# Kernel tuning notes

Hardware: AMD Instinct MI355X
Metric: run time of the kernel (lower is better)

## Reference

```python
import jax, jax.numpy as jnp
import numpy as np

N, E, F_IN, H, K = 50000, 800000, 64, 128, 4


def setup_inputs() -> dict:
    key = jax.random.key(0)
    k0, k1, k2, k3 = jax.random.split(key, 4)
    features = jax.random.normal(k0, (N, F_IN), dtype=jnp.float32)
    edge_index = jax.random.randint(k1, (2, E), 0, N, dtype=jnp.int32)
    # ChebConv parameters: one [F_IN, H] weight per Chebyshev order + shared bias
    cheb_w = jax.random.normal(k2, (K, F_IN, H), dtype=jnp.float32) * 0.05
    cheb_b = jnp.zeros((H,), dtype=jnp.float32)
    # final Linear(H, 1)
    final_w = jax.random.normal(k3, (H, 1), dtype=jnp.float32) * 0.05
    final_b = jnp.zeros((1,), dtype=jnp.float32)
    return dict(features=features, edge_index=edge_index, cheb_w=cheb_w,
                cheb_b=cheb_b, final_w=final_w, final_b=final_b)


def _cheb_conv(x, edge_index, w, b):
    # PyG ChebConv, sym normalization, lambda_max = 2.0, no self-loops in input:
    # L_hat = (2/lambda_max) * (I - D^-1/2 A D^-1/2) - I = -D^-1/2 A D^-1/2
    row, col = edge_index[0], edge_index[1]
    n = x.shape[0]
    deg = jax.ops.segment_sum(jnp.ones((row.shape[0],), dtype=x.dtype), row,
                              num_segments=n)
    dinv = jnp.where(deg > 0, jax.lax.rsqrt(jnp.maximum(deg, 1e-12)), 0.0)
    ew = -dinv[row] * dinv[col]  # [E] normalized (negated) edge weights

    def spmm(z):  # L_hat @ z via gather-multiply-scatter
        return jax.ops.segment_sum(z[col] * ew[:, None], row, num_segments=n)

    Tx0 = x
    out = Tx0 @ w[0]
    Tx1 = spmm(Tx0)
    if w.shape[0] > 1:
        out = out + Tx1 @ w[1]
    for k in range(2, w.shape[0]):  # Chebyshev recursion T_k = 2 L T_{k-1} - T_{k-2}
        Tx2 = 2.0 * spmm(Tx1) - Tx0
        out = out + Tx2 @ w[k]
        Tx0, Tx1 = Tx1, Tx2
    return out + b


def reference(features, edge_index, cheb_w, cheb_b, final_w, final_b):
    h = jnp.tanh(_cheb_conv(features, edge_index, cheb_w, cheb_b))  # [N, H]
    return (h @ final_w + final_b).reshape(-1)  # [N]
```

## Files before the change

### kernel.cpp

```cpp
#include <hip/hip_runtime.h>
#include <hip/hip_fp16.h>
#include <math.h>


#define FIN 64
#define HDIM 128

typedef _Float16 half8 __attribute__((ext_vector_type(8)));
typedef float f32x4 __attribute__((ext_vector_type(4)));

union U16 { uint4 u; __half2 h2[4]; half8 h8; };

__global__ void count_deg(const int* __restrict__ row, int* __restrict__ deg, int E) {
    int e = blockIdx.x * blockDim.x + threadIdx.x;
    if (e < E) atomicAdd(&deg[row[e]], 1);
}

__global__ void make_dinv(const int* __restrict__ deg, float* __restrict__ dinv, int n) {
    int i = blockIdx.x * blockDim.x + threadIdx.x;
    if (i < n) {
        int d = deg[i];
        dinv[i] = (d > 0) ? rsqrtf((float)d) : 0.f;
    }
}

__global__ void cvt_feat(const float4* __restrict__ src, uint4* __restrict__ dst, int n8) {
    int i = blockIdx.x * blockDim.x + threadIdx.x;
    if (i >= n8) return;
    float4 a = src[i * 2], b = src[i * 2 + 1];
    U16 v;
    v.h2[0] = __float22half2_rn(make_float2(a.x, a.y));
    v.h2[1] = __float22half2_rn(make_float2(a.z, a.w));
    v.h2[2] = __float22half2_rn(make_float2(b.x, b.y));
    v.h2[3] = __float22half2_rn(make_float2(b.z, b.w));
    dst[i] = v.u;
}

__global__ void make_bfrag(const float* __restrict__ W, uint4* __restrict__ bfrag) {
    int t = blockIdx.x * blockDim.x + threadIdx.x;
    if (t >= 8 * 8 * 64) return;
    int lane = t & 63;
    int ht = (t >> 6) & 7;
    int kk = t >> 9;
    int h = ht * 16 + (lane & 15);
    int kb = kk * 32 + (lane >> 4) * 8;
    U16 v;
#pragma unroll
    for (int j = 0; j < 4; ++j) {
        float a = W[(kb + 2 * j) * HDIM + h];
        float b = W[(kb + 2 * j + 1) * HDIM + h];
        v.h2[j] = __float22half2_rn(make_float2(a, b));
    }
    bfrag[t] = v.u;
}

__global__ void scan_local(const int* __restrict__ in, int* __restrict__ out,
                           int* __restrict__ bsum, int n) {
    __shared__ int buf[1024];
    int tid = threadIdx.x;
    int gid = blockIdx.x * 1024 + tid;
    int v = (gid < n) ? in[gid] : 0;
    int x = v;
    buf[tid] = x;
    __syncthreads();
    for (int off = 1; off < 1024; off <<= 1) {
        int t = (tid >= off) ? buf[tid - off] : 0;
        __syncthreads();
        x += t;
        buf[tid] = x;
        __syncthreads();
    }
    if (gid < n) out[gid] = x - v;
    if (tid == 1023) bsum[blockIdx.x] = x;
}

__global__ void scan_bsums(int* bsum, int nb) {
    if (blockIdx.x == 0 && threadIdx.x == 0) {
        int acc = 0;
        for (int b = 0; b < nb; ++b) { int t = bsum[b]; bsum[b] = acc; acc += t; }
    }
}

__global__ void scan_finish(int* __restrict__ rowptr, const int* __restrict__ bsum,
                            int* __restrict__ cursor, int n, int E) {
    int i = blockIdx.x * blockDim.x + threadIdx.x;
    if (i < n) {
        int v = rowptr[i] + bsum[i >> 10];
        rowptr[i] = v;
        cursor[i] = v;
    } else if (i == n) {
        rowptr[n] = E;
    }
}

__global__ void scatter_edges(const int* __restrict__ row, const int* __restrict__ col,
                              const float* __restrict__ dinv, int* __restrict__ cursor,
                              int2* __restrict__ epk, int E) {
    int e = blockIdx.x * blockDim.x + threadIdx.x;
    if (e < E) {
        int r = row[e], c = col[e];
        int p = atomicAdd(&cursor[r], 1);
        float w = -dinv[r] * dinv[c];
        epk[p] = make_int2(c, __float_as_int(w));
    }
}

__global__ __launch_bounds__(256) void spmm_h(
        const int* __restrict__ rowptr, const int2* __restrict__ epk,
        const uint4* __restrict__ in8, const uint4* __restrict__ prev8,
        float scale, uint4* __restrict__ out8, int n) {
    int lane = threadIdx.x & 63;
    int wid = (blockIdx.x * blockDim.x + threadIdx.x) >> 6;
    int li = lane & 7, g = lane >> 3;
    int r = wid * 8 + g;
    if (r >= n) return;
    int s = rowptr[r], e = rowptr[r + 1];
    float acc[8];
#pragma unroll
    for (int j = 0; j < 8; ++j) acc[j] = 0.f;
    int p = s;
    for (; p + 4 <= e; p += 4) {
        int2 m0 = epk[p], m1 = epk[p + 1], m2 = epk[p + 2], m3 = epk[p + 3];
        U16 v0, v1, v2, v3;
        v0.u = in8[(size_t)m0.x * 8 + li];
        v1.u = in8[(size_t)m1.x * 8 + li];
        v2.u = in8[(size_t)m2.x * 8 + li];
        v3.u = in8[(size_t)m3.x * 8 + li];
        float w0 = __int_as_float(m0.y), w1 = __int_as_float(m1.y);
        float w2 = __int_as_float(m2.y), w3 = __int_as_float(m3.y);
#pragma unroll
        for (int j = 0; j < 4; ++j) {
            float2 f0 = __half22float2(v0.h2[j]);
            float2 f1 = __half22float2(v1.h2[j]);
            float2 f2 = __half22float2(v2.h2[j]);
            float2 f3 = __half22float2(v3.h2[j]);
            acc[2 * j]     = fmaf(w0, f0.x, acc[2 * j]);
            acc[2 * j + 1] = fmaf(w0, f0.y, acc[2 * j + 1]);
            acc[2 * j]     = fmaf(w1, f1.x, acc[2 * j]);
            acc[2 * j + 1] = fmaf(w1, f1.y, acc[2 * j + 1]);
            acc[2 * j]     = fmaf(w2, f2.x, acc[2 * j]);
            acc[2 * j + 1] = fmaf(w2, f2.y, acc[2 * j + 1]);
            acc[2 * j]     = fmaf(w3, f3.x, acc[2 * j]);
            acc[2 * j + 1] = fmaf(w3, f3.y, acc[2 * j + 1]);
        }
    }
    for (; p < e; ++p) {
        int2 m0 = epk[p];
        U16 v0;
        v0.u = in8[(size_t)m0.x * 8 + li];
        float w0 = __int_as_float(m0.y);
#pragma unroll
        for (int j = 0; j < 4; ++j) {
            float2 f0 = __half22float2(v0.h2[j]);
            acc[2 * j]     = fmaf(w0, f0.x, acc[2 * j]);
            acc[2 * j + 1] = fmaf(w0, f0.y, acc[2 * j + 1]);
        }
    }
    if (prev8) {
        U16 pv;
        pv.u = prev8[(size_t)r * 8 + li];
#pragma unroll
        for (int j = 0; j < 4; ++j) {
            float2 f = __half22float2(pv.h2[j]);
            acc[2 * j]     = fmaf(scale, acc[2 * j], -f.x);
            acc[2 * j + 1] = fmaf(scale, acc[2 * j + 1], -f.y);
        }
    }
    U16 res;
#pragma unroll
    for (int j = 0; j < 4; ++j)
        res.h2[j] = __float22half2_rn(make_float2(acc[2 * j], acc[2 * j + 1]));
    out8[(size_t)r * 8 + li] = res.u;
}

__device__ inline float tanh_fast(float x) {
    x = fmaxf(-10.f, fminf(10.f, x));
    float e = __expf(2.f * x);
    return (e - 1.f) / (e + 1.f);
}

__global__ __launch_bounds__(256) void gemm_mfma(
        const uint4* __restrict__ tx0, const uint4* __restrict__ tx1,
        const uint4* __restrict__ tx2, const uint4* __restrict__ tx3,
        const uint4* __restrict__ bfrag,
        const float* __restrict__ cheb_b, const float* __restrict__ fw,
        const float* __restrict__ fb, float* __restrict__ out, int n) {
    int tid = threadIdx.x;
    int lane = tid & 63;
    int wave = tid >> 6;
    int q = lane >> 4, m = lane & 15;
    int node_base = blockIdx.x * 64 + wave * 16;
    int node = node_base + m;
    size_t nd = (node < n) ? (size_t)node : 0;

    f32x4 acc[8];
#pragma unroll
    for (int t = 0; t < 8; ++t) acc[t] = (f32x4){0.f, 0.f, 0.f, 0.f};

    const uint4* txs[4] = {tx0, tx1, tx2, tx3};
#pragma unroll
    for (int kk = 0; kk < 8; ++kk) {
        U16 av;
        av.u = txs[kk >> 1][nd * 8 + (kk & 1) * 4 + q];
#pragma unroll
        for (int ht = 0; ht < 8; ++ht) {
            U16 bv;
            bv.u = bfrag[(kk * 8 + ht) * 64 + lane];
            acc[ht] = __builtin_amdgcn_mfma_f32_16x16x32_f16(av.h8, bv.h8, acc[ht], 0, 0, 0);
        }
    }

    float s[4] = {0.f, 0.f, 0.f, 0.f};
#pragma unroll
    for (int ht = 0; ht < 8; ++ht) {
        int h = ht * 16 + m;
        float cb = cheb_b[h];
        float fv = fw[h];
#pragma unroll
        for (int r = 0; r < 4; ++r)
            s[r] = fmaf(tanh_fast(acc[ht][r] + cb), fv, s[r]);
    }
#pragma unroll
    for (int r = 0; r < 4; ++r) {
        for (int msk = 1; msk < 16; msk <<= 1)
            s[r] += __shfl_xor(s[r], msk, 64);
    }
    if (m == 0) {
        float fb0 = fb[0];
#pragma unroll
        for (int r = 0; r < 4; ++r) {
            int o = node_base + q * 4 + r;
            if (o < n) out[o] = s[r] + fb0;
        }
    }
}

extern "C" void kernel_launch(void* const* d_in, const int* in_sizes, int n_in,
                              void* d_out, int out_size, void* d_ws, size_t ws_size,
                              hipStream_t stream) {
    const float* features = (const float*)d_in[0];
    const int*   edge_index = (const int*)d_in[1];
    const float* cheb_w  = (const float*)d_in[2];
    const float* cheb_b  = (const float*)d_in[3];
    const float* final_w = (const float*)d_in[4];
    const float* final_b = (const float*)d_in[5];
    int N = in_sizes[0] / FIN;
    int E = in_sizes[1] / 2;
    const int* row = edge_index;
    const int* col = edge_index + E;

    char* p = (char*)d_ws;
    auto alloc = [&](size_t bytes) {
        char* r = p;
        p += (bytes + 255) & ~(size_t)255;
        return r;
    };
    int*   deg    = (int*)alloc((size_t)N * 4);
    float* dinv   = (float*)alloc((size_t)N * 4);
    int*   rowptr = (int*)alloc((size_t)(N + 1) * 4);
    int*   cursor = (int*)alloc((size_t)N * 4);
    int*   bsum   = (int*)alloc(1024 * 4);
    int2*  epk    = (int2*)alloc((size_t)E * 8);
    uint4* feath  = (uint4*)alloc((size_t)N * FIN * 2);
    uint4* tx1h   = (uint4*)alloc((size_t)N * FIN * 2);
    uint4* tx2h   = (uint4*)alloc((size_t)N * FIN * 2);
    uint4* tx3h   = (uint4*)alloc((size_t)N * FIN * 2);
    uint4* bfrag  = (uint4*)alloc(4096 * 16);

    hipMemsetAsync(deg, 0, (size_t)N * 4, stream);
    count_deg<<<(E + 255) / 256, 256, 0, stream>>>(row, deg, E);
    make_dinv<<<(N + 255) / 256, 256, 0, stream>>>(deg, dinv, N);
    int n8 = N * FIN / 8;
    cvt_feat<<<(n8 + 255) / 256, 256, 0, stream>>>((const float4*)features, feath, n8);
    make_bfrag<<<16, 256, 0, stream>>>(cheb_w, bfrag);
    int nb = (N + 1023) / 1024;
    scan_local<<<nb, 1024, 0, stream>>>(deg, rowptr, bsum, N);
    scan_bsums<<<1, 64, 0, stream>>>(bsum, nb);
    scan_finish<<<(N + 1 + 255) / 256, 256, 0, stream>>>(rowptr, bsum, cursor, N, E);
    scatter_edges<<<(E + 255) / 256, 256, 0, stream>>>(row, col, dinv, cursor, epk, E);

    int waves = (N + 7) / 8;
    int spmm_blocks = (waves * 64 + 255) / 256;
    spmm_h<<<spmm_blocks, 256, 0, stream>>>(rowptr, epk, feath, nullptr, 1.f, tx1h, N);
    spmm_h<<<spmm_blocks, 256, 0, stream>>>(rowptr, epk, tx1h, feath, 2.f, tx2h, N);
    spmm_h<<<spmm_blocks, 256, 0, stream>>>(rowptr, epk, tx2h, tx1h, 2.f, tx3h, N);

    gemm_mfma<<<(N + 63) / 64, 256, 0, stream>>>(feath, tx1h, tx2h, tx3h, bfrag,
                                                 cheb_b, final_w, final_b,
                                                 (float*)d_out, N);
}
```

Baseline: 231.7 us.

## Split SpMM rows across edge halves and feature halves with shuffle reduction

```diff
diff --git a/kernel.cpp b/kernel.cpp
--- a/kernel.cpp
+++ b/kernel.cpp
@@ -109,23 +109,33 @@
         const int* __restrict__ rowptr, const int2* __restrict__ epk,
         const uint4* __restrict__ in8, const uint4* __restrict__ prev8,
         float scale, uint4* __restrict__ out8, int n) {
-    int lane = threadIdx.x & 63;
-    int wid = (blockIdx.x * blockDim.x + threadIdx.x) >> 6;
-    int li = lane & 7, g = lane >> 3;
-    int r = wid * 8 + g;
+    int half = blockIdx.x & 1;
+    int bid = blockIdx.x >> 1;
+    int tid = threadIdx.x;
+    int lane = tid & 63;
+    int wave = bid * 4 + (tid >> 6);
+    int g = lane >> 3;
+    int sub = (lane >> 2) & 1;
+    int li = lane & 3;
+    int r = wave * 8 + g;
     if (r >= n) return;
     int s = rowptr[r], e = rowptr[r + 1];
+    int mid = s + ((e - s + 1) >> 1);
+    int p = sub ? mid : s;
+    int pe = sub ? e : mid;
+    int fo = half * 4 + li;
+
     float acc[8];
 #pragma unroll
     for (int j = 0; j < 8; ++j) acc[j] = 0.f;
-    int p = s;
-    for (; p + 4 <= e; p += 4) {
+
+    for (; p + 4 <= pe; p += 4) {
         int2 m0 = epk[p], m1 = epk[p + 1], m2 = epk[p + 2], m3 = epk[p + 3];
         U16 v0, v1, v2, v3;
-        v0.u = in8[(size_t)m0.x * 8 + li];
-        v1.u = in8[(size_t)m1.x * 8 + li];
-        v2.u = in8[(size_t)m2.x * 8 + li];
-        v3.u = in8[(size_t)m3.x * 8 + li];
+        v0.u = in8[(size_t)m0.x * 8 + fo];
+        v1.u = in8[(size_t)m1.x * 8 + fo];
+        v2.u = in8[(size_t)m2.x * 8 + fo];
+        v3.u = in8[(size_t)m3.x * 8 + fo];
         float w0 = __int_as_float(m0.y), w1 = __int_as_float(m1.y);
         float w2 = __int_as_float(m2.y), w3 = __int_as_float(m3.y);
 #pragma unroll
@@ -144,10 +154,10 @@
             acc[2 * j + 1] = fmaf(w3, f3.y, acc[2 * j + 1]);
         }
     }
-    for (; p < e; ++p) {
+    for (; p < pe; ++p) {
         int2 m0 = epk[p];
         U16 v0;
-        v0.u = in8[(size_t)m0.x * 8 + li];
+        v0.u = in8[(size_t)m0.x * 8 + fo];
         float w0 = __int_as_float(m0.y);
 #pragma unroll
         for (int j = 0; j < 4; ++j) {
@@ -156,21 +166,29 @@
             acc[2 * j + 1] = fmaf(w0, f0.y, acc[2 * j + 1]);
         }
     }
-    if (prev8) {
-        U16 pv;
-        pv.u = prev8[(size_t)r * 8 + li];
-#pragma unroll
-        for (int j = 0; j < 4; ++j) {
-            float2 f = __half22float2(pv.h2[j]);
-            acc[2 * j]     = fmaf(scale, acc[2 * j], -f.x);
-            acc[2 * j + 1] = fmaf(scale, acc[2 * j + 1], -f.y);
-        }
-    }
-    U16 res;
-#pragma unroll
-    for (int j = 0; j < 4; ++j)
-        res.h2[j] = __float22half2_rn(make_float2(acc[2 * j], acc[2 * j + 1]));
-    out8[(size_t)r * 8 + li] = res.u;
+#pragma unroll
+    for (int j = 0; j < 8; ++j) acc[j] += __shfl_xor(acc[j], 4, 64);
+
+    if (sub == 0) {
+        if (prev8) {
+            U16 pv;
+            pv.u = prev8[(size_t)r * 8 + fo];
+#pragma unroll
+            for (int j = 0; j < 4; ++j) {
+                float2 f = __half22float2(pv.h2[j]);
+                acc[2 * j]     = fmaf(scale, acc[2 * j], -f.x);
+                acc[2 * j + 1] = fmaf(scale, acc[2 * j + 1], -f.y);
+            }
+        } else {
+#pragma unroll
+            for (int j = 0; j < 8; ++j) acc[j] *= scale;
+        }
+        U16 res;
+#pragma unroll
+        for (int j = 0; j < 4; ++j)
+            res.h2[j] = __float22half2_rn(make_float2(acc[2 * j], acc[2 * j + 1]));
+        out8[(size_t)r * 8 + fo] = res.u;
+    }
 }
 
 __device__ inline float tanh_fast(float x) {
@@ -279,11 +297,11 @@
     scan_finish<<<(N + 1 + 255) / 256, 256, 0, stream>>>(rowptr, bsum, cursor, N, E);
     scatter_edges<<<(E + 255) / 256, 256, 0, stream>>>(row, col, dinv, cursor, epk, E);
 
-    int waves = (N + 7) / 8;
-    int spmm_blocks = (waves * 64 + 255) / 256;
-    spmm_h<<<spmm_blocks, 256, 0, stream>>>(rowptr, epk, feath, nullptr, 1.f, tx1h, N);
-    spmm_h<<<spmm_blocks, 256, 0, stream>>>(rowptr, epk, tx1h, feath, 2.f, tx2h, N);
-    spmm_h<<<spmm_blocks, 256, 0, stream>>>(rowptr, epk, tx2h, tx1h, 2.f, tx3h, N);
+    int blocks_per_half = (N + 31) / 32;
+    int spmm_grid = blocks_per_half * 2;
+    spmm_h<<<spmm_grid, 256, 0, stream>>>(rowptr, epk, feath, nullptr, 1.f, tx1h, N);
+    spmm_h<<<spmm_grid, 256, 0, stream>>>(rowptr, epk, tx1h, feath, 2.f, tx2h, N);
+    spmm_h<<<spmm_grid, 256, 0, stream>>>(rowptr, epk, tx2h, tx1h, 2.f, tx3h, N);
 
     gemm_mfma<<<(N + 63) / 64, 256, 0, stream>>>(feath, tx1h, tx2h, tx3h, bfrag,
                                                  cheb_b, final_w, final_b,
```

Result: slower. 261.0 us (+12.7%).

## Factor symmetric normalization out of SpMM and store column-only CSR

Applied to the files above, without the earlier changes.

```diff
diff --git a/kernel.cpp b/kernel.cpp
--- a/kernel.cpp
+++ b/kernel.cpp
@@ -24,16 +24,23 @@
     }
 }
 
-__global__ void cvt_feat(const float4* __restrict__ src, uint4* __restrict__ dst, int n8) {
+__global__ void cvt_feat(const float4* __restrict__ src, const float* __restrict__ dinv,
+                         uint4* __restrict__ dsth, uint4* __restrict__ dsts, int n8) {
     int i = blockIdx.x * blockDim.x + threadIdx.x;
     if (i >= n8) return;
+    float d = dinv[i >> 3];
     float4 a = src[i * 2], b = src[i * 2 + 1];
-    U16 v;
+    U16 v, vs;
     v.h2[0] = __float22half2_rn(make_float2(a.x, a.y));
     v.h2[1] = __float22half2_rn(make_float2(a.z, a.w));
     v.h2[2] = __float22half2_rn(make_float2(b.x, b.y));
     v.h2[3] = __float22half2_rn(make_float2(b.z, b.w));
-    dst[i] = v.u;
+    vs.h2[0] = __float22half2_rn(make_float2(d * a.x, d * a.y));
+    vs.h2[1] = __float22half2_rn(make_float2(d * a.z, d * a.w));
+    vs.h2[2] = __float22half2_rn(make_float2(d * b.x, d * b.y));
+    vs.h2[3] = __float22half2_rn(make_float2(d * b.z, d * b.w));
+    dsth[i] = v.u;
+    dsts[i] = vs.u;
 }
 
 __global__ void make_bfrag(const float* __restrict__ W, uint4* __restrict__ bfrag) {
@@ -93,22 +100,24 @@
     }
 }
 
-__global__ void scatter_edges(const int* __restrict__ row, const int* __restrict__ col,
-                              const float* __restrict__ dinv, int* __restrict__ cursor,
-                              int2* __restrict__ epk, int E) {
+__global__ void scatter_pass(const int* __restrict__ row, const int* __restrict__ col,
+                             int* __restrict__ cursor, int* __restrict__ col_s,
+                             int E, int r_lo, int r_hi) {
     int e = blockIdx.x * blockDim.x + threadIdx.x;
     if (e < E) {
-        int r = row[e], c = col[e];
-        int p = atomicAdd(&cursor[r], 1);
-        float w = -dinv[r] * dinv[c];
-        epk[p] = make_int2(c, __float_as_int(w));
-    }
-}
-
-__global__ __launch_bounds__(256) void spmm_h(
-        const int* __restrict__ rowptr, const int2* __restrict__ epk,
-        const uint4* __restrict__ in8, const uint4* __restrict__ prev8,
-        float scale, uint4* __restrict__ out8, int n) {
+        int r = row[e];
+        if (r >= r_lo && r < r_hi) {
+            int p = atomicAdd(&cursor[r], 1);
+            col_s[p] = col[e];
+        }
+    }
+}
+
+__global__ __launch_bounds__(256) void spmm_g(
+        const int* __restrict__ rowptr, const int* __restrict__ cols,
+        const uint4* __restrict__ ins, const uint4* __restrict__ prevu,
+        const float* __restrict__ dinv, float two,
+        uint4* __restrict__ outu, uint4* __restrict__ outs, int n) {
     int lane = threadIdx.x & 63;
     int wid = (blockIdx.x * blockDim.x + threadIdx.x) >> 6;
     int li = lane & 7, g = lane >> 3;
@@ -119,58 +128,61 @@
 #pragma unroll
     for (int j = 0; j < 8; ++j) acc[j] = 0.f;
     int p = s;
-    for (; p + 4 <= e; p += 4) {
-        int2 m0 = epk[p], m1 = epk[p + 1], m2 = epk[p + 2], m3 = epk[p + 3];
-        U16 v0, v1, v2, v3;
-        v0.u = in8[(size_t)m0.x * 8 + li];
-        v1.u = in8[(size_t)m1.x * 8 + li];
-        v2.u = in8[(size_t)m2.x * 8 + li];
-        v3.u = in8[(size_t)m3.x * 8 + li];
-        float w0 = __int_as_float(m0.y), w1 = __int_as_float(m1.y);
-        float w2 = __int_as_float(m2.y), w3 = __int_as_float(m3.y);
-#pragma unroll
-        for (int j = 0; j < 4; ++j) {
-            float2 f0 = __half22float2(v0.h2[j]);
-            float2 f1 = __half22float2(v1.h2[j]);
-            float2 f2 = __half22float2(v2.h2[j]);
-            float2 f3 = __half22float2(v3.h2[j]);
-            acc[2 * j]     = fmaf(w0, f0.x, acc[2 * j]);
-            acc[2 * j + 1] = fmaf(w0, f0.y, acc[2 * j + 1]);
-            acc[2 * j]     = fmaf(w1, f1.x, acc[2 * j]);
-            acc[2 * j + 1] = fmaf(w1, f1.y, acc[2 * j + 1]);
-            acc[2 * j]     = fmaf(w2, f2.x, acc[2 * j]);
-            acc[2 * j + 1] = fmaf(w2, f2.y, acc[2 * j + 1]);
-            acc[2 * j]     = fmaf(w3, f3.x, acc[2 * j]);
-            acc[2 * j + 1] = fmaf(w3, f3.y, acc[2 * j + 1]);
+    for (; p + 8 <= e; p += 8) {
+        int c[8];
+#pragma unroll
+        for (int j = 0; j < 8; ++j) c[j] = cols[p + j];
+        U16 v[8];
+#pragma unroll
+        for (int j = 0; j < 8; ++j) v[j].u = ins[(size_t)c[j] * 8 + li];
+#pragma unroll
+        for (int j = 0; j < 8; ++j) {
+#pragma unroll
+            for (int t = 0; t < 4; ++t) {
+                float2 f = __half22float2(v[j].h2[t]);
+                acc[2 * t] += f.x;
+                acc[2 * t + 1] += f.y;
+            }
         }
     }
     for (; p < e; ++p) {
-        int2 m0 = epk[p];
-        U16 v0;
-        v0.u = in8[(size_t)m0.x * 8 + li];
-        float w0 = __int_as_float(m0.y);
-#pragma unroll
-        for (int j = 0; j < 4; ++j) {
-            float2 f0 = __half22float2(v0.h2[j]);
-            acc[2 * j]     = fmaf(w0, f0.x, acc[2 * j]);
-            acc[2 * j + 1] = fmaf(w0, f0.y, acc[2 * j + 1]);
-        }
-    }
-    if (prev8) {
+        U16 v;
+        v.u = ins[(size_t)cols[p] * 8 + li];
+#pragma unroll
+        for (int t = 0; t < 4; ++t) {
+            float2 f = __half22float2(v.h2[t]);
+            acc[2 * t] += f.x;
+            acc[2 * t + 1] += f.y;
+        }
+    }
+    float d = dinv[r];
+    float rs = -d * two;
+    float res[8];
+    if (prevu) {
         U16 pv;
-        pv.u = prev8[(size_t)r * 8 + li];
-#pragma unroll
-        for (int j = 0; j < 4; ++j) {
-            float2 f = __half22float2(pv.h2[j]);
-            acc[2 * j]     = fmaf(scale, acc[2 * j], -f.x);
-            acc[2 * j + 1] = fmaf(scale, acc[2 * j + 1], -f.y);
-        }
-    }
-    U16 res;
-#pragma unroll
-    for (int j = 0; j < 4; ++j)
-        res.h2[j] = __float22half2_rn(make_float2(acc[2 * j], acc[2 * j + 1]));
-    out8[(size_t)r * 8 + li] = res.u;
+        pv.u = prevu[(size_t)r * 8 + li];
+#pragma unroll
+        for (int t = 0; t < 4; ++t) {
+            float2 f = __half22float2(pv.h2[t]);
+            res[2 * t]     = fmaf(rs, acc[2 * t], -f.x);
+            res[2 * t + 1] = fmaf(rs, acc[2 * t + 1], -f.y);
+        }
+    } else {
+#pragma unroll
+        for (int j = 0; j < 8; ++j) res[j] = rs * acc[j];
+    }
+    U16 ru;
+#pragma unroll
+    for (int t = 0; t < 4; ++t)
+        ru.h2[t] = __float22half2_rn(make_float2(res[2 * t], res[2 * t + 1]));
+    outu[(size_t)r * 8 + li] = ru.u;
+    if (outs) {
+        U16 rsv;
+#pragma unroll
+        for (int t = 0; t < 4; ++t)
+            rsv.h2[t] = __float22half2_rn(make_float2(d * res[2 * t], d * res[2 * t + 1]));
+        outs[(size_t)r * 8 + li] = rsv.u;
+    }
 }
 
 __device__ inline float tanh_fast(float x) {
@@ -260,10 +272,13 @@
     int*   rowptr = (int*)alloc((size_t)(N + 1) * 4);
     int*   cursor = (int*)alloc((size_t)N * 4);
     int*   bsum   = (int*)alloc(1024 * 4);
-    int2*  epk    = (int2*)alloc((size_t)E * 8);
+    int*   col_s  = (int*)alloc((size_t)E * 4);
     uint4* feath  = (uint4*)alloc((size_t)N * FIN * 2);
+    uint4* feats  = (uint4*)alloc((size_t)N * FIN * 2);
     uint4* tx1h   = (uint4*)alloc((size_t)N * FIN * 2);
+    uint4* tx1s   = (uint4*)alloc((size_t)N * FIN * 2);
     uint4* tx2h   = (uint4*)alloc((size_t)N * FIN * 2);
+    uint4* tx2s   = (uint4*)alloc((size_t)N * FIN * 2);
     uint4* tx3h   = (uint4*)alloc((size_t)N * FIN * 2);
     uint4* bfrag  = (uint4*)alloc(4096 * 16);
 
@@ -271,19 +286,29 @@
     count_deg<<<(E + 255) / 256, 256, 0, stream>>>(row, deg, E);
     make_dinv<<<(N + 255) / 256, 256, 0, stream>>>(deg, dinv, N);
     int n8 = N * FIN / 8;
-    cvt_feat<<<(n8 + 255) / 256, 256, 0, stream>>>((const float4*)features, feath, n8);
+    cvt_feat<<<(n8 + 255) / 256, 256, 0, stream>>>((const float4*)features, dinv,
+                                                   feath, feats, n8);
     make_bfrag<<<16, 256, 0, stream>>>(cheb_w, bfrag);
     int nb = (N + 1023) / 1024;
     scan_local<<<nb, 1024, 0, stream>>>(deg, rowptr, bsum, N);
     scan_bsums<<<1, 64, 0, stream>>>(bsum, nb);
     scan_finish<<<(N + 1 + 255) / 256, 256, 0, stream>>>(rowptr, bsum, cursor, N, E);
-    scatter_edges<<<(E + 255) / 256, 256, 0, stream>>>(row, col, dinv, cursor, epk, E);
-
-    int waves = (N + 7) / 8;
-    int spmm_blocks = (waves * 64 + 255) / 256;
-    spmm_h<<<spmm_blocks, 256, 0, stream>>>(rowptr, epk, feath, nullptr, 1.f, tx1h, N);
-    spmm_h<<<spmm_blocks, 256, 0, stream>>>(rowptr, epk, tx1h, feath, 2.f, tx2h, N);
-    spmm_h<<<spmm_blocks, 256, 0, stream>>>(rowptr, epk, tx2h, tx1h, 2.f, tx3h, N);
+
+    int eb = (E + 255) / 256;
+    int stride = (N + 3) / 4;
+    for (int pass = 0; pass < 4; ++pass) {
+        int lo = pass * stride;
+        int hi = (pass == 3) ? N : lo + stride;
+        scatter_pass<<<eb, 256, 0, stream>>>(row, col, cursor, col_s, E, lo, hi);
+    }
+
+    int spmm_blocks = (((N + 7) / 8) * 64 + 255) / 256;
+    spmm_g<<<spmm_blocks, 256, 0, stream>>>(rowptr, col_s, feats, nullptr, dinv,
+                                            1.f, tx1h, tx1s, N);
+    spmm_g<<<spmm_blocks, 256, 0, stream>>>(rowptr, col_s, tx1s, feath, dinv,
+                                            2.f, tx2h, tx2s, N);
+    spmm_g<<<spmm_blocks, 256, 0, stream>>>(rowptr, col_s, tx2s, tx1h, dinv,
+                                            2.f, tx3h, nullptr, N);
 
     gemm_mfma<<<(N + 63) / 64, 256, 0, stream>>>(feath, tx1h, tx2h, tx3h, bfrag,
                                                  cheb_b, final_w, final_b,
```

After: 257.4 us. 1.11x slower.
